# Kernel tuning notes

Hardware: AMD Instinct MI355X
Metric: run time of the kernel (lower is better)

## Reference

```python
import jax, jax.numpy as jnp
import numpy as np


def setup_inputs() -> dict:
    key = jax.random.key(0)
    ks = jax.random.split(key, 7)
    B, C, W, H = 4, 256, 64, 64
    C8 = C // 8
    return {
        "x": jax.random.normal(ks[0], (B, C, W, H), dtype=jnp.float32),
        "Wq": jax.random.normal(ks[1], (C8, C), dtype=jnp.float32) * 0.05,
        "bq": jax.random.normal(ks[2], (C8,), dtype=jnp.float32) * 0.05,
        "Wk": jax.random.normal(ks[3], (C8, C), dtype=jnp.float32) * 0.05,
        "bk": jax.random.normal(ks[4], (C8,), dtype=jnp.float32) * 0.05,
        "Wv": jax.random.normal(ks[5], (C, C), dtype=jnp.float32) * 0.05,
        "bv": jax.random.normal(ks[6], (C,), dtype=jnp.float32) * 0.05,
    }


def reference(x, Wq, bq, Wk, bk, Wv, bv):
    B, C, W, H = x.shape
    N = W * H
    xf = x.reshape(B, C, N)  # flatten spatial dims
    # 1x1 convs == per-position linear projections
    q = jnp.einsum('oc,bcn->bno', Wq, xf) + bq            # (B, N, C/8)
    k = jnp.einsum('oc,bcn->bon', Wk, xf) + bk[None, :, None]  # (B, C/8, N)
    # attention scores (B, N, N); original applies softmax over dim=1
    attn = jax.nn.softmax(jnp.einsum('bno,bom->bnm', q, k), axis=1)
    v = jnp.einsum('oc,bcn->bno', Wv, xf) + bv            # (B, N, C)
    out = jnp.einsum('bnm,bmc->bnc', attn, v)             # (B, N, C)
    # faithful to original: raw view of (B, N, C) as (B, C, W, H)
    return out.reshape(B, C, W, H)
```

## Files before the change

kernel.cpp:

```cpp
#include <hip/hip_runtime.h>
#include <math.h>

#define NB 4
#define CC 256
#define CO 32
#define NN 4096
#define MU 320
#define LOG2E 1.44269504088896f

typedef __attribute__((ext_vector_type(4))) float f4;
typedef __attribute__((ext_vector_type(8))) short s8;
typedef __attribute__((ext_vector_type(8))) unsigned short us8;
typedef __attribute__((ext_vector_type(2))) unsigned int u2;
typedef __attribute__((ext_vector_type(4))) unsigned int u4i;

__device__ __forceinline__ unsigned short f2bf(float f) {
    unsigned int u = __float_as_uint(f);
    u = (u + 0x7FFFu + ((u >> 16) & 1u)) >> 16;
    return (unsigned short)u;
}
__device__ __forceinline__ unsigned int cvtpk(float lo, float hi) {
    unsigned int r;
    asm("v_cvt_pk_bf16_f32 %0, %1, %2" : "=v"(r) : "v"(lo), "v"(hi));
    return r;
}
__device__ __forceinline__ int swz128(int row, int colByte) {
    return row * 128 + (colByte ^ ((row & 7) << 4));
}

union s8u4 { s8 s; u4i u; };

__global__ __launch_bounds__(256) void prepw_kernel(
    const float* __restrict__ Wq, const float* __restrict__ bq,
    const float* __restrict__ Wk, const float* __restrict__ bk,
    const float* __restrict__ Wv, const float* __restrict__ bv,
    unsigned short* __restrict__ Wb, float* __restrict__ fb)
{
    const int t = threadIdx.x;
    #pragma unroll
    for (int i = 0; i < 4; ++i) {
        const int e = blockIdx.x * 1024 + i * 256 + t;
        const int u = e >> 8, c = e & 255;
        float val = (u < 32) ? Wq[u * 256 + c]
                  : (u < 64) ? Wk[(u - 32) * 256 + c]
                             : Wv[(u - 64) * 256 + c];
        Wb[e] = f2bf(val);
    }
    if (blockIdx.x == 0) {
        for (int u = t; u < MU; u += 256)
            fb[u] = (u < 32) ? bq[u] : (u < 64) ? bk[u - 32] : bv[u - 64];
    }
}

__global__ __launch_bounds__(256) void projf_kernel(
    const float* __restrict__ x, const unsigned short* __restrict__ Wb,
    const float* __restrict__ fb,
    unsigned short* __restrict__ qb, unsigned short* __restrict__ kb,
    unsigned short* __restrict__ vtb)
{
    __shared__ float xl[32][260];

    const int t   = threadIdx.x;
    const int b   = blockIdx.x >> 7;
    const int nbl = blockIdx.x & 127;
    const int n0  = nbl * 32;

    {
        const int nl = t & 7;
        const int c8 = t >> 3;
        #pragma unroll
        for (int pass = 0; pass < 8; ++pass) {
            const int c = c8 + pass * 32;
            f4 xv = *reinterpret_cast<const f4*>(x + ((size_t)(b * CC + c)) * NN + n0 + nl * 4);
            #pragma unroll
            for (int j = 0; j < 4; ++j) xl[nl * 4 + j][c] = xv[j];
        }
    }
    __syncthreads();

    const int w    = t >> 6;
    const int l    = t & 63;
    const int l15  = l & 15;
    const int g4   = l >> 4;
    const int nw   = w & 1;
    const int uw   = w >> 1;
    const int nloc = nw * 16 + l15;
    const int n    = n0 + nloc;

    s8 bfr[8];
    #pragma unroll
    for (int kk = 0; kk < 8; ++kk) {
        f4 a  = *reinterpret_cast<const f4*>(&xl[nloc][kk * 32 + g4 * 8]);
        f4 c2 = *reinterpret_cast<const f4*>(&xl[nloc][kk * 32 + g4 * 8 + 4]);
        s8u4 tmp;
        tmp.u = (u4i){ cvtpk(a[0], a[1]), cvtpk(a[2], a[3]),
                       cvtpk(c2[0], c2[1]), cvtpk(c2[2], c2[3]) };
        bfr[kk] = tmp.s;
    }

    const f4 z = {0.f, 0.f, 0.f, 0.f};
    unsigned short* qrow = qb + ((size_t)(b * NN + n)) * CO;
    unsigned short* krow = kb + ((size_t)(b * NN + n)) * CO;

    #pragma unroll
    for (int i = 0; i < 10; ++i) {
        const int u0 = (uw * 10 + i) * 16;
        f4 acc = z;
        #pragma unroll
        for (int kk = 0; kk < 8; ++kk) {
            s8 af = *reinterpret_cast<const s8*>(Wb + (size_t)(u0 + l15) * CC + kk * 32 + g4 * 8);
            acc = __builtin_amdgcn_mfma_f32_16x16x32_bf16(af, bfr[kk], acc, 0, 0, 0);
        }
        f4 bias4 = *reinterpret_cast<const f4*>(fb + u0 + g4 * 4);
        if (u0 < 32) {
            u2 pw = { cvtpk((acc[0] + bias4[0]) * LOG2E, (acc[1] + bias4[1]) * LOG2E),
                      cvtpk((acc[2] + bias4[2]) * LOG2E, (acc[3] + bias4[3]) * LOG2E) };
            *reinterpret_cast<u2*>(qrow + u0 + g4 * 4) = pw;
        } else if (u0 < 64) {
            u2 pw = { cvtpk(acc[0] + bias4[0], acc[1] + bias4[1]),
                      cvtpk(acc[2] + bias4[2], acc[3] + bias4[3]) };
            *reinterpret_cast<u2*>(krow + (u0 - 32) + g4 * 4) = pw;
        } else {
            const int cbase = u0 - 64 + g4 * 4;
            #pragma unroll
            for (int r = 0; r < 4; ++r)
                vtb[((size_t)(b * CC + cbase + r)) * NN + n] = f2bf(acc[r] + bias4[r]);
        }
    }
}

__global__ __launch_bounds__(256) void colstats_kernel(
    const unsigned short* __restrict__ qb, const unsigned short* __restrict__ kb,
    const unsigned short* __restrict__ vtb, unsigned short* __restrict__ vfr)
{
    __shared__ float red[4][16];
    __shared__ float civl[16];

    const int t   = threadIdx.x;
    const int b   = blockIdx.x >> 8;
    const int mb  = blockIdx.x & 255;
    const int l   = t & 63;
    const int w   = t >> 6;
    const int l15 = l & 15;
    const int g4  = l >> 4;
    const int m   = mb * 16 + l15;

    const unsigned short* qbB = qb + (size_t)b * NN * CO;
    s8 kfrag = *reinterpret_cast<const s8*>(kb + ((size_t)b * NN + m) * CO + g4 * 8);

    const f4 z = {0.f, 0.f, 0.f, 0.f};
    float ssum = 0.f;

    const int nbeg = w * 1024, nend = nbeg + 1024;
    for (int n0 = nbeg; n0 < nend; n0 += 32) {
        s8 a0 = *reinterpret_cast<const s8*>(qbB + (size_t)(n0 + l15) * CO + g4 * 8);
        s8 a1 = *reinterpret_cast<const s8*>(qbB + (size_t)(n0 + 16 + l15) * CO + g4 * 8);
        f4 d0 = __builtin_amdgcn_mfma_f32_16x16x32_bf16(a0, kfrag, z, 0, 0, 0);
        f4 d1 = __builtin_amdgcn_mfma_f32_16x16x32_bf16(a1, kfrag, z, 0, 0, 0);
        #pragma unroll
        for (int r = 0; r < 4; ++r) ssum += exp2f(d0[r]) + exp2f(d1[r]);
    }

    ssum += __shfl_xor(ssum, 16);
    ssum += __shfl_xor(ssum, 32);
    if (l < 16) red[w][l15] = ssum;
    __syncthreads();
    if (w == 0 && l < 16)
        civl[l15] = 1.0f / (red[0][l15] + red[1][l15] + red[2][l15] + red[3][l15]);
    __syncthreads();

    const int mt   = mb >> 2;
    const int ksl  = (mb >> 1) & 1;
    const int g4b  = (mb & 1) * 2;
    const int cg   = t >> 4;
    const int l15v = t & 15;
    const unsigned short* vp = vtb + ((size_t)(b * CC + t)) * NN + mb * 16;
    unsigned short* dst = vfr + (size_t)b * 1048576
                        + (((mt * 16 + cg) * 2 + ksl) << 9)
                        + (g4b * 16 + l15v) * 8;
    #pragma unroll
    for (int i = 0; i < 2; ++i) {
        us8 vv = *reinterpret_cast<const us8*>(vp + i * 8);
        u4i o;
        #pragma unroll
        for (int e2 = 0; e2 < 4; ++e2) {
            float f0 = __uint_as_float((unsigned int)vv[2 * e2]     << 16) * civl[i * 8 + 2 * e2];
            float f1 = __uint_as_float((unsigned int)vv[2 * e2 + 1] << 16) * civl[i * 8 + 2 * e2 + 1];
            o[e2] = cvtpk(f0, f1);
        }
        *reinterpret_cast<u4i*>(dst + i * 128) = o;
    }
}

__global__ __launch_bounds__(512) void attn_kernel(
    const unsigned short* __restrict__ qb, const unsigned short* __restrict__ kb,
    const unsigned short* __restrict__ vfr, float* __restrict__ out)
{
    __shared__ __align__(16) char plds[2][64 * 128];

    const int t    = threadIdx.x;
    const int bid  = blockIdx.x;
    const int cblk = bid & 1;
    const int nblk = (bid >> 1) & 63;
    const int b    = bid >> 7;
    const int n0   = nblk * 64;
    const int c0   = cblk * 128;
    const int l    = t & 63;
    const int w    = t >> 6;
    const int l15  = l & 15;
    const int g4   = l >> 4;
    const int g    = w >> 1;
    const int p    = w & 1;
    const int wrn  = w >> 2;
    const int wcq  = w & 3;

    const unsigned short* qbB = qb  + (size_t)b * NN * CO;
    const unsigned short* kbB = kb  + (size_t)b * NN * CO;

    s8 qfrag = *reinterpret_cast<const s8*>(qbB + (size_t)(n0 + g * 16 + l15) * CO + g4 * 8);

    const int pw0  = swz128(g * 16 + l15, (2 * p) * 32 + g4 * 8);
    const int pw1  = swz128(g * 16 + l15, (2 * p + 1) * 32 + g4 * 8);
    const int prk0a0 = swz128(wrn * 32 +      l15,      g4 * 16);
    const int prk0a1 = swz128(wrn * 32 + 16 + l15,      g4 * 16);
    const int prk1a0 = swz128(wrn * 32 +      l15, 64 + g4 * 16);
    const int prk1a1 = swz128(wrn * 32 + 16 + l15, 64 + g4 * 16);

    const unsigned short* kp  = kbB + (size_t)((2 * p) * 16 + l15) * CO + g4 * 8;
    const unsigned short* vpf = vfr + (size_t)b * 1048576
                              + (size_t)((c0 >> 4) + wcq * 2) * 1024 + l * 8;

    s8 kreg[2];
    s8 vA0, vA1, vA2, vA3, vB0, vB1, vB2, vB3;
    const f4 z = {0.f, 0.f, 0.f, 0.f};

#define LOADK() do { \
        kreg[0] = *reinterpret_cast<const s8*>(kp); \
        kreg[1] = *reinterpret_cast<const s8*>(kp + 16 * CO); \
        kp += 64 * CO; \
    } while (0)

#define LOADVB(V0, V1, V2, V3) do { \
        V0 = *reinterpret_cast<const s8*>(vpf); \
        V1 = *reinterpret_cast<const s8*>(vpf + 512); \
        V2 = *reinterpret_cast<const s8*>(vpf + 1024); \
        V3 = *reinterpret_cast<const s8*>(vpf + 1536); \
        vpf += 16384; \
    } while (0)

#define STAGE(BUF) do { \
        f4 d0 = __builtin_amdgcn_mfma_f32_16x16x32_bf16(kreg[0], qfrag, z, 0, 0, 0); \
        f4 d1 = __builtin_amdgcn_mfma_f32_16x16x32_bf16(kreg[1], qfrag, z, 0, 0, 0); \
        u2 pq0 = { cvtpk(exp2f(d0[0]), exp2f(d0[1])), cvtpk(exp2f(d0[2]), exp2f(d0[3])) }; \
        u2 pq1 = { cvtpk(exp2f(d1[0]), exp2f(d1[1])), cvtpk(exp2f(d1[2]), exp2f(d1[3])) }; \
        *reinterpret_cast<u2*>(plds[BUF] + pw0) = pq0; \
        *reinterpret_cast<u2*>(plds[BUF] + pw1) = pq1; \
    } while (0)

#define PVSTEP(BUF, V0, V1, V2, V3) do { \
        s8 pa00 = *reinterpret_cast<const s8*>(plds[BUF] + prk0a0); \
        s8 pa01 = *reinterpret_cast<const s8*>(plds[BUF] + prk0a1); \
        s8 pa10 = *reinterpret_cast<const s8*>(plds[BUF] + prk1a0); \
        s8 pa11 = *reinterpret_cast<const s8*>(plds[BUF] + prk1a1); \
        __builtin_amdgcn_s_setprio(1); \
        acc[0][0] = __builtin_amdgcn_mfma_f32_16x16x32_bf16(pa00, V0, acc[0][0], 0, 0, 0); \
        acc[0][1] = __builtin_amdgcn_mfma_f32_16x16x32_bf16(pa00, V2, acc[0][1], 0, 0, 0); \
        acc[1][0] = __builtin_amdgcn_mfma_f32_16x16x32_bf16(pa01, V0, acc[1][0], 0, 0, 0); \
        acc[1][1] = __builtin_amdgcn_mfma_f32_16x16x32_bf16(pa01, V2, acc[1][1], 0, 0, 0); \
        acc[0][0] = __builtin_amdgcn_mfma_f32_16x16x32_bf16(pa10, V1, acc[0][0], 0, 0, 0); \
        acc[0][1] = __builtin_amdgcn_mfma_f32_16x16x32_bf16(pa10, V3, acc[0][1], 0, 0, 0); \
        acc[1][0] = __builtin_amdgcn_mfma_f32_16x16x32_bf16(pa11, V1, acc[1][0], 0, 0, 0); \
        acc[1][1] = __builtin_amdgcn_mfma_f32_16x16x32_bf16(pa11, V3, acc[1][1], 0, 0, 0); \
        __builtin_amdgcn_s_setprio(0); \
    } while (0)

    f4 acc[2][2];
    acc[0][0] = z; acc[0][1] = z; acc[1][0] = z; acc[1][1] = z;

    LOADK();
    LOADVB(vA0, vA1, vA2, vA3);
    STAGE(0);
    LOADK();
    LOADVB(vB0, vB1, vB2, vB3);
    __syncthreads();

    for (int i = 0; i < 64; i += 2) {
        if (i < 63) {
            STAGE(1);
            if (i < 62) LOADK();
        }
        PVSTEP(0, vA0, vA1, vA2, vA3);
        if (i < 62) LOADVB(vA0, vA1, vA2, vA3);
        __syncthreads();

        if (i + 1 < 63) {
            STAGE(0);
            if (i + 1 < 62) LOADK();
        }
        PVSTEP(1, vB0, vB1, vB2, vB3);
        if (i + 1 < 62) LOADVB(vB0, vB1, vB2, vB3);
        __syncthreads();
    }

#undef LOADK
#undef LOADVB
#undef STAGE
#undef PVSTEP

    #pragma unroll
    for (int a = 0; a < 2; ++a) {
        const int row = n0 + wrn * 32 + a * 16 + g4 * 4;
        #pragma unroll
        for (int c = 0; c < 2; ++c) {
            const int col = c0 + wcq * 32 + c * 16 + l15;
            #pragma unroll
            for (int r = 0; r < 4; ++r)
                out[((size_t)(b * NN + row + r)) * CC + col] = acc[a][c][r];
        }
    }
}

extern "C" void kernel_launch(void* const* d_in, const int* in_sizes, int n_in,
                              void* d_out, int out_size, void* d_ws, size_t ws_size,
                              hipStream_t stream)
{
    const float* x  = (const float*)d_in[0];
    const float* Wq = (const float*)d_in[1];
    const float* bq = (const float*)d_in[2];
    const float* Wk = (const float*)d_in[3];
    const float* bk = (const float*)d_in[4];
    const float* Wv = (const float*)d_in[5];
    const float* bv = (const float*)d_in[6];
    float* out = (float*)d_out;

    unsigned short* qb  = (unsigned short*)d_ws;
    unsigned short* kb  = qb  + (size_t)NB * NN * CO;
    unsigned short* vtb = kb  + (size_t)NB * NN * CO;
    unsigned short* vfr = vtb + (size_t)NB * CC * NN;
    unsigned short* Wb  = vfr + (size_t)NB * CC * NN;
    float*          fb  = (float*)(Wb + (size_t)MU * CC);

    prepw_kernel<<<dim3(80), dim3(256), 0, stream>>>(Wq, bq, Wk, bk, Wv, bv, Wb, fb);
    projf_kernel<<<dim3(512), dim3(256), 0, stream>>>(x, Wb, fb, qb, kb, vtb);
    colstats_kernel<<<dim3(1024), dim3(256), 0, stream>>>(qb, kb, vtb, vfr);
    attn_kernel<<<dim3(512), dim3(512), 0, stream>>>(qb, kb, vfr, out);
}
```

Before: 122.3 us.

## Give each wave an independent 32x64 attention tile with private LDS and no block barriers

The attention kernel is restructured so each wave owns a 32-row by 64-channel output tile. Each wave computes its own score tile, exponentiates it, and stages it through a private padded LDS region, which removes all __syncthreads. The PV MFMAs swap operand order so results can be stored as float4 rows, and the grid is halved to 256 blocks of 512 threads. In exchange each wave recomputes the QK scores for its column chunk (four-way redundancy across channel chunks) and holds more registers, which limits occupancy.

```diff
diff --git a/kernel.cpp b/kernel.cpp
--- a/kernel.cpp
+++ b/kernel.cpp
@@ -23,9 +23,6 @@
     unsigned int r;
     asm("v_cvt_pk_bf16_f32 %0, %1, %2" : "=v"(r) : "v"(lo), "v"(hi));
     return r;
-}
-__device__ __forceinline__ int swz128(int row, int colByte) {
-    return row * 128 + (colByte ^ ((row & 7) << 4));
 }
 
 union s8u4 { s8 s; u4i u; };
@@ -192,131 +189,158 @@
     }
 }
 
-__global__ __launch_bounds__(512) void attn_kernel(
+__global__ __launch_bounds__(512, 2) void attn_kernel(
     const unsigned short* __restrict__ qb, const unsigned short* __restrict__ kb,
     const unsigned short* __restrict__ vfr, float* __restrict__ out)
 {
-    __shared__ __align__(16) char plds[2][64 * 128];
+    __shared__ __align__(16) char plds[8][32 * 144];
 
     const int t    = threadIdx.x;
-    const int bid  = blockIdx.x;
-    const int cblk = bid & 1;
-    const int nblk = (bid >> 1) & 63;
-    const int b    = bid >> 7;
-    const int n0   = nblk * 64;
-    const int c0   = cblk * 128;
+    const int w    = t >> 6;
     const int l    = t & 63;
-    const int w    = t >> 6;
     const int l15  = l & 15;
     const int g4   = l >> 4;
-    const int g    = w >> 1;
-    const int p    = w & 1;
-    const int wrn  = w >> 2;
-    const int wcq  = w & 3;
-
-    const unsigned short* qbB = qb  + (size_t)b * NN * CO;
-    const unsigned short* kbB = kb  + (size_t)b * NN * CO;
-
-    s8 qfrag = *reinterpret_cast<const s8*>(qbB + (size_t)(n0 + g * 16 + l15) * CO + g4 * 8);
-
-    const int pw0  = swz128(g * 16 + l15, (2 * p) * 32 + g4 * 8);
-    const int pw1  = swz128(g * 16 + l15, (2 * p + 1) * 32 + g4 * 8);
-    const int prk0a0 = swz128(wrn * 32 +      l15,      g4 * 16);
-    const int prk0a1 = swz128(wrn * 32 + 16 + l15,      g4 * 16);
-    const int prk1a0 = swz128(wrn * 32 +      l15, 64 + g4 * 16);
-    const int prk1a1 = swz128(wrn * 32 + 16 + l15, 64 + g4 * 16);
-
-    const unsigned short* kp  = kbB + (size_t)((2 * p) * 16 + l15) * CO + g4 * 8;
-    const unsigned short* vpf = vfr + (size_t)b * 1048576
-                              + (size_t)((c0 >> 4) + wcq * 2) * 1024 + l * 8;
-
-    s8 kreg[2];
-    s8 vA0, vA1, vA2, vA3, vB0, vB1, vB2, vB3;
+    const int bid  = blockIdx.x;
+    const int b    = bid >> 6;
+    const int rem  = bid & 63;
+    const int chunk = rem * 8 + w;
+    const int ch   = chunk & 3;
+    const int nc   = chunk >> 2;
+    const int n0   = nc * 32;
+    const int c0   = ch * 64;
+
+    const unsigned short* qbB = qb + (size_t)b * NN * CO;
+    const unsigned short* kbB = kb + (size_t)b * NN * CO;
+
+    s8 qf0 = *reinterpret_cast<const s8*>(qbB + (size_t)(n0 + l15) * CO + g4 * 8);
+    s8 qf1 = *reinterpret_cast<const s8*>(qbB + (size_t)(n0 + 16 + l15) * CO + g4 * 8);
+
+    char* pbase = plds[w];
+    const int pwr = l15 * 144 + g4 * 8;
+    const int pw00 = pwr,              pw01 = pwr + 32,  pw02 = pwr + 64,  pw03 = pwr + 96;
+    const int pw10 = pwr + 2304,       pw11 = pw10 + 32, pw12 = pw10 + 64, pw13 = pw10 + 96;
+    const int prr = l15 * 144 + g4 * 16;
+    const int pr00 = prr,        pr01 = prr + 64;
+    const int pr10 = prr + 2304, pr11 = pr10 + 64;
+
+    const unsigned short* kpA = kbB + (size_t)l15 * CO + g4 * 8;
+    const unsigned short* kpB = kpA + (size_t)64 * CO;
+    const unsigned short* vpA = vfr + (size_t)b * 1048576 + ch * 4096 + l * 8;
+    const unsigned short* vpB = vpA + 16384;
+
+    s8 kA0, kA1, kA2, kA3, kB0, kB1, kB2, kB3;
+    s8 vA[8], vB[8];
     const f4 z = {0.f, 0.f, 0.f, 0.f};
 
-#define LOADK() do { \
-        kreg[0] = *reinterpret_cast<const s8*>(kp); \
-        kreg[1] = *reinterpret_cast<const s8*>(kp + 16 * CO); \
-        kp += 64 * CO; \
-    } while (0)
-
-#define LOADVB(V0, V1, V2, V3) do { \
-        V0 = *reinterpret_cast<const s8*>(vpf); \
-        V1 = *reinterpret_cast<const s8*>(vpf + 512); \
-        V2 = *reinterpret_cast<const s8*>(vpf + 1024); \
-        V3 = *reinterpret_cast<const s8*>(vpf + 1536); \
-        vpf += 16384; \
-    } while (0)
-
-#define STAGE(BUF) do { \
-        f4 d0 = __builtin_amdgcn_mfma_f32_16x16x32_bf16(kreg[0], qfrag, z, 0, 0, 0); \
-        f4 d1 = __builtin_amdgcn_mfma_f32_16x16x32_bf16(kreg[1], qfrag, z, 0, 0, 0); \
-        u2 pq0 = { cvtpk(exp2f(d0[0]), exp2f(d0[1])), cvtpk(exp2f(d0[2]), exp2f(d0[3])) }; \
-        u2 pq1 = { cvtpk(exp2f(d1[0]), exp2f(d1[1])), cvtpk(exp2f(d1[2]), exp2f(d1[3])) }; \
-        *reinterpret_cast<u2*>(plds[BUF] + pw0) = pq0; \
-        *reinterpret_cast<u2*>(plds[BUF] + pw1) = pq1; \
-    } while (0)
-
-#define PVSTEP(BUF, V0, V1, V2, V3) do { \
-        s8 pa00 = *reinterpret_cast<const s8*>(plds[BUF] + prk0a0); \
-        s8 pa01 = *reinterpret_cast<const s8*>(plds[BUF] + prk0a1); \
-        s8 pa10 = *reinterpret_cast<const s8*>(plds[BUF] + prk1a0); \
-        s8 pa11 = *reinterpret_cast<const s8*>(plds[BUF] + prk1a1); \
+#define LOADKA() do { \
+        kA0 = *reinterpret_cast<const s8*>(kpA); \
+        kA1 = *reinterpret_cast<const s8*>(kpA + 512); \
+        kA2 = *reinterpret_cast<const s8*>(kpA + 1024); \
+        kA3 = *reinterpret_cast<const s8*>(kpA + 1536); \
+        kpA += 4096; \
+    } while (0)
+#define LOADKB() do { \
+        kB0 = *reinterpret_cast<const s8*>(kpB); \
+        kB1 = *reinterpret_cast<const s8*>(kpB + 512); \
+        kB2 = *reinterpret_cast<const s8*>(kpB + 1024); \
+        kB3 = *reinterpret_cast<const s8*>(kpB + 1536); \
+        kpB += 4096; \
+    } while (0)
+#define LOADVA() do { \
+        vA[0] = *reinterpret_cast<const s8*>(vpA); \
+        vA[1] = *reinterpret_cast<const s8*>(vpA + 512); \
+        vA[2] = *reinterpret_cast<const s8*>(vpA + 1024); \
+        vA[3] = *reinterpret_cast<const s8*>(vpA + 1536); \
+        vA[4] = *reinterpret_cast<const s8*>(vpA + 2048); \
+        vA[5] = *reinterpret_cast<const s8*>(vpA + 2560); \
+        vA[6] = *reinterpret_cast<const s8*>(vpA + 3072); \
+        vA[7] = *reinterpret_cast<const s8*>(vpA + 3584); \
+        vpA += 32768; \
+    } while (0)
+#define LOADVB() do { \
+        vB[0] = *reinterpret_cast<const s8*>(vpB); \
+        vB[1] = *reinterpret_cast<const s8*>(vpB + 512); \
+        vB[2] = *reinterpret_cast<const s8*>(vpB + 1024); \
+        vB[3] = *reinterpret_cast<const s8*>(vpB + 1536); \
+        vB[4] = *reinterpret_cast<const s8*>(vpB + 2048); \
+        vB[5] = *reinterpret_cast<const s8*>(vpB + 2560); \
+        vB[6] = *reinterpret_cast<const s8*>(vpB + 3072); \
+        vB[7] = *reinterpret_cast<const s8*>(vpB + 3584); \
+        vpB += 32768; \
+    } while (0)
+
+#define TILE(K0, K1, K2, K3, V) do { \
+        f4 d0 = __builtin_amdgcn_mfma_f32_16x16x32_bf16(K0, qf0, z, 0, 0, 0); \
+        f4 d1 = __builtin_amdgcn_mfma_f32_16x16x32_bf16(K1, qf0, z, 0, 0, 0); \
+        f4 d2 = __builtin_amdgcn_mfma_f32_16x16x32_bf16(K2, qf0, z, 0, 0, 0); \
+        f4 d3 = __builtin_amdgcn_mfma_f32_16x16x32_bf16(K3, qf0, z, 0, 0, 0); \
+        *reinterpret_cast<u2*>(pbase + pw00) = (u2){ cvtpk(exp2f(d0[0]), exp2f(d0[1])), cvtpk(exp2f(d0[2]), exp2f(d0[3])) }; \
+        *reinterpret_cast<u2*>(pbase + pw01) = (u2){ cvtpk(exp2f(d1[0]), exp2f(d1[1])), cvtpk(exp2f(d1[2]), exp2f(d1[3])) }; \
+        *reinterpret_cast<u2*>(pbase + pw02) = (u2){ cvtpk(exp2f(d2[0]), exp2f(d2[1])), cvtpk(exp2f(d2[2]), exp2f(d2[3])) }; \
+        *reinterpret_cast<u2*>(pbase + pw03) = (u2){ cvtpk(exp2f(d3[0]), exp2f(d3[1])), cvtpk(exp2f(d3[2]), exp2f(d3[3])) }; \
+        d0 = __builtin_amdgcn_mfma_f32_16x16x32_bf16(K0, qf1, z, 0, 0, 0); \
+        d1 = __builtin_amdgcn_mfma_f32_16x16x32_bf16(K1, qf1, z, 0, 0, 0); \
+        d2 = __builtin_amdgcn_mfma_f32_16x16x32_bf16(K2, qf1, z, 0, 0, 0); \
+        d3 = __builtin_amdgcn_mfma_f32_16x16x32_bf16(K3, qf1, z, 0, 0, 0); \
+        *reinterpret_cast<u2*>(pbase + pw10) = (u2){ cvtpk(exp2f(d0[0]), exp2f(d0[1])), cvtpk(exp2f(d0[2]), exp2f(d0[3])) }; \
+        *reinterpret_cast<u2*>(pbase + pw11) = (u2){ cvtpk(exp2f(d1[0]), exp2f(d1[1])), cvtpk(exp2f(d1[2]), exp2f(d1[3])) }; \
+        *reinterpret_cast<u2*>(pbase + pw12) = (u2){ cvtpk(exp2f(d2[0]), exp2f(d2[1])), cvtpk(exp2f(d2[2]), exp2f(d2[3])) }; \
+        *reinterpret_cast<u2*>(pbase + pw13) = (u2){ cvtpk(exp2f(d3[0]), exp2f(d3[1])), cvtpk(exp2f(d3[2]), exp2f(d3[3])) }; \
+        s8 p00 = *reinterpret_cast<const s8*>(pbase + pr00); \
+        s8 p01 = *reinterpret_cast<const s8*>(pbase + pr01); \
+        s8 p10 = *reinterpret_cast<const s8*>(pbase + pr10); \
+        s8 p11 = *reinterpret_cast<const s8*>(pbase + pr11); \
         __builtin_amdgcn_s_setprio(1); \
-        acc[0][0] = __builtin_amdgcn_mfma_f32_16x16x32_bf16(pa00, V0, acc[0][0], 0, 0, 0); \
-        acc[0][1] = __builtin_amdgcn_mfma_f32_16x16x32_bf16(pa00, V2, acc[0][1], 0, 0, 0); \
-        acc[1][0] = __builtin_amdgcn_mfma_f32_16x16x32_bf16(pa01, V0, acc[1][0], 0, 0, 0); \
-        acc[1][1] = __builtin_amdgcn_mfma_f32_16x16x32_bf16(pa01, V2, acc[1][1], 0, 0, 0); \
-        acc[0][0] = __builtin_amdgcn_mfma_f32_16x16x32_bf16(pa10, V1, acc[0][0], 0, 0, 0); \
-        acc[0][1] = __builtin_amdgcn_mfma_f32_16x16x32_bf16(pa10, V3, acc[0][1], 0, 0, 0); \
-        acc[1][0] = __builtin_amdgcn_mfma_f32_16x16x32_bf16(pa11, V1, acc[1][0], 0, 0, 0); \
-        acc[1][1] = __builtin_amdgcn_mfma_f32_16x16x32_bf16(pa11, V3, acc[1][1], 0, 0, 0); \
+        acc00 = __builtin_amdgcn_mfma_f32_16x16x32_bf16(V[0], p00, acc00, 0, 0, 0); \
+        acc01 = __builtin_amdgcn_mfma_f32_16x16x32_bf16(V[2], p00, acc01, 0, 0, 0); \
+        acc02 = __builtin_amdgcn_mfma_f32_16x16x32_bf16(V[4], p00, acc02, 0, 0, 0); \
+        acc03 = __builtin_amdgcn_mfma_f32_16x16x32_bf16(V[6], p00, acc03, 0, 0, 0); \
+        acc10 = __builtin_amdgcn_mfma_f32_16x16x32_bf16(V[0], p10, acc10, 0, 0, 0); \
+        acc11 = __builtin_amdgcn_mfma_f32_16x16x32_bf16(V[2], p10, acc11, 0, 0, 0); \
+        acc12 = __builtin_amdgcn_mfma_f32_16x16x32_bf16(V[4], p10, acc12, 0, 0, 0); \
+        acc13 = __builtin_amdgcn_mfma_f32_16x16x32_bf16(V[6], p10, acc13, 0, 0, 0); \
+        acc00 = __builtin_amdgcn_mfma_f32_16x16x32_bf16(V[1], p01, acc00, 0, 0, 0); \
+        acc01 = __builtin_amdgcn_mfma_f32_16x16x32_bf16(V[3], p01, acc01, 0, 0, 0); \
+        acc02 = __builtin_amdgcn_mfma_f32_16x16x32_bf16(V[5], p01, acc02, 0, 0, 0); \
+        acc03 = __builtin_amdgcn_mfma_f32_16x16x32_bf16(V[7], p01, acc03, 0, 0, 0); \
+        acc10 = __builtin_amdgcn_mfma_f32_16x16x32_bf16(V[1], p11, acc10, 0, 0, 0); \
+        acc11 = __builtin_amdgcn_mfma_f32_16x16x32_bf16(V[3], p11, acc11, 0, 0, 0); \
+        acc12 = __builtin_amdgcn_mfma_f32_16x16x32_bf16(V[5], p11, acc12, 0, 0, 0); \
+        acc13 = __builtin_amdgcn_mfma_f32_16x16x32_bf16(V[7], p11, acc13, 0, 0, 0); \
         __builtin_amdgcn_s_setprio(0); \
     } while (0)
 
-    f4 acc[2][2];
-    acc[0][0] = z; acc[0][1] = z; acc[1][0] = z; acc[1][1] = z;
-
-    LOADK();
-    LOADVB(vA0, vA1, vA2, vA3);
-    STAGE(0);
-    LOADK();
-    LOADVB(vB0, vB1, vB2, vB3);
-    __syncthreads();
+    f4 acc00 = z, acc01 = z, acc02 = z, acc03 = z;
+    f4 acc10 = z, acc11 = z, acc12 = z, acc13 = z;
+
+    LOADKA(); LOADVA();
+    LOADKB(); LOADVB();
 
     for (int i = 0; i < 64; i += 2) {
-        if (i < 63) {
-            STAGE(1);
-            if (i < 62) LOADK();
-        }
-        PVSTEP(0, vA0, vA1, vA2, vA3);
-        if (i < 62) LOADVB(vA0, vA1, vA2, vA3);
-        __syncthreads();
-
-        if (i + 1 < 63) {
-            STAGE(0);
-            if (i + 1 < 62) LOADK();
-        }
-        PVSTEP(1, vB0, vB1, vB2, vB3);
-        if (i + 1 < 62) LOADVB(vB0, vB1, vB2, vB3);
-        __syncthreads();
-    }
-
-#undef LOADK
+        TILE(kA0, kA1, kA2, kA3, vA);
+        if (i + 2 < 64) { LOADKA(); LOADVA(); }
+        TILE(kB0, kB1, kB2, kB3, vB);
+        if (i + 3 < 64) { LOADKB(); LOADVB(); }
+    }
+
+#undef LOADKA
+#undef LOADKB
+#undef LOADVA
 #undef LOADVB
-#undef STAGE
-#undef PVSTEP
-
-    #pragma unroll
-    for (int a = 0; a < 2; ++a) {
-        const int row = n0 + wrn * 32 + a * 16 + g4 * 4;
-        #pragma unroll
-        for (int c = 0; c < 2; ++c) {
-            const int col = c0 + wcq * 32 + c * 16 + l15;
-            #pragma unroll
-            for (int r = 0; r < 4; ++r)
-                out[((size_t)(b * NN + row + r)) * CC + col] = acc[a][c][r];
-        }
+#undef TILE
+
+    float* outB = out + (size_t)b * NN * CC;
+    #pragma unroll
+    for (int h = 0; h < 2; ++h) {
+        float* orow = outB + (size_t)(n0 + h * 16 + l15) * CC + c0 + g4 * 4;
+        f4 a0 = h ? acc10 : acc00;
+        f4 a1 = h ? acc11 : acc01;
+        f4 a2 = h ? acc12 : acc02;
+        f4 a3 = h ? acc13 : acc03;
+        *reinterpret_cast<f4*>(orow)      = a0;
+        *reinterpret_cast<f4*>(orow + 16) = a1;
+        *reinterpret_cast<f4*>(orow + 32) = a2;
+        *reinterpret_cast<f4*>(orow + 48) = a3;
     }
 }
 
@@ -343,5 +367,5 @@
     prepw_kernel<<<dim3(80), dim3(256), 0, stream>>>(Wq, bq, Wk, bk, Wv, bv, Wb, fb);
     projf_kernel<<<dim3(512), dim3(256), 0, stream>>>(x, Wb, fb, qb, kb, vtb);
     colstats_kernel<<<dim3(1024), dim3(256), 0, stream>>>(qb, kb, vtb, vfr);
-    attn_kernel<<<dim3(512), dim3(512), 0, stream>>>(qb, kb, vfr, out);
-}
+    attn_kernel<<<dim3(256), dim3(512), 0, stream>>>(qb, kb, vfr, out);
+}
```

After: 144.4 us. 18.1% more time.
